# Kernel optimization log

Measured on AMD Instinct MI355X. Metric: run time of the kernel, lower is better.

The kernel has to match this reference:

```python
import jax, jax.numpy as jnp
import numpy as np

D_MODEL = 2048
D_LATENT = 512


def setup_inputs() -> dict:
    key = jax.random.key(0)
    ks = jax.random.split(key, 6)
    x = jax.random.normal(ks[0], (2, 4096, D_MODEL), dtype=jnp.float32)
    cache = jax.random.normal(ks[1], (2, 4096, D_LATENT), dtype=jnp.float32)
    s = 0.02
    # weights stored (in_features, out_features); equivalent to torch Linear (no bias)
    W_kv = jax.random.normal(ks[2], (D_MODEL, D_LATENT), dtype=jnp.float32) * s
    W_q = jax.random.normal(ks[3], (D_MODEL, D_MODEL), dtype=jnp.float32) * s
    W_lq = jax.random.normal(ks[4], (D_MODEL, D_LATENT), dtype=jnp.float32) * s
    W_o = jax.random.normal(ks[5], (D_LATENT, D_MODEL), dtype=jnp.float32) * s
    return {"x": x, "cache": cache, "W_kv": W_kv, "W_q": W_q, "W_lq": W_lq, "W_o": W_o}


def reference(x, cache, W_kv, W_q, W_lq, W_o):
    # latent compression of inputs: (B, S, d_latent)
    l_kv_new = jnp.einsum('bsd,dl->bsl', x, W_kv)
    # query path: x -> query (d_model) -> latent query (d_latent)
    q = jnp.einsum('bsd,de->bse', x, W_q)
    lq = jnp.einsum('bse,el->bsl', q, W_lq)
    # append to cache: (B, T+S, d_latent)
    l_kv = jnp.concatenate([cache, l_kv_new], axis=1)
    scale = jnp.sqrt(jnp.float32(D_LATENT)).astype(x.dtype)
    # attention in latent space: scores (B, S, T+S)
    scores = jnp.einsum('bsl,btl->bst', lq, l_kv) / scale
    weights = jax.nn.softmax(scores, axis=-1)
    ctx = jnp.einsum('bst,btl->bsl', weights, l_kv)
    out = jnp.einsum('bsl,ld->bsd', ctx, W_o)
    return out, l_kv
```

## Files before the change

### kernel.cpp

```cpp
#include <hip/hip_runtime.h>
#include <hip/hip_bf16.h>
#include <math.h>


typedef _Float16 f16x8 __attribute__((ext_vector_type(8)));
typedef _Float16 f16x4 __attribute__((ext_vector_type(4)));
typedef float    f32x4 __attribute__((ext_vector_type(4)));
typedef float    f32x8 __attribute__((ext_vector_type(8)));

__device__ __forceinline__ void gl_lds16(const void* g, void* l) {
  __builtin_amdgcn_global_load_lds(
      (const __attribute__((address_space(1))) void*)g,
      (__attribute__((address_space(3))) void*)l, 16, 0, 0);
}


__global__ __launch_bounds__(256) void k_cvt(const float* __restrict__ in,
                                             _Float16* __restrict__ out, int n4) {
  int i = blockIdx.x * blockDim.x + threadIdx.x;
  int st = gridDim.x * blockDim.x;
  for (; i < n4; i += st) {
    f32x4 v = reinterpret_cast<const f32x4*>(in)[i];
    reinterpret_cast<f16x4*>(out)[i] = __builtin_convertvector(v, f16x4);
  }
}

__global__ __launch_bounds__(256) void k_cache(const float* __restrict__ cache,
                                               float* __restrict__ lkv_f32,
                                               _Float16* __restrict__ lkv16, int n4) {
  int i = blockIdx.x * blockDim.x + threadIdx.x;
  int st = gridDim.x * blockDim.x;
  for (; i < n4; i += st) {
    f32x4 v = reinterpret_cast<const f32x4*>(cache)[i];
    int e = i << 2;
    int b = e >> 21;
    int dst = e + (b << 21);
    *reinterpret_cast<f32x4*>(lkv_f32 + dst) = v;
    *reinterpret_cast<f16x4*>(lkv16 + dst) = __builtin_convertvector(v, f16x4);
  }
}

__global__ __launch_bounds__(256) void k_tc(const float* __restrict__ in,
                                            _Float16* __restrict__ out, int R, int C) {
  __shared__ float t[32][33];
  const int c0 = blockIdx.x << 5, r0 = blockIdx.y << 5;
  const int tid = threadIdx.x;
  {
    int r = tid >> 3, c4 = (tid & 7) << 2;
    f32x4 v = *reinterpret_cast<const f32x4*>(&in[(long)(r0 + r) * C + c0 + c4]);
    t[r][c4] = v[0]; t[r][c4 + 1] = v[1]; t[r][c4 + 2] = v[2]; t[r][c4 + 3] = v[3];
  }
  __syncthreads();
  {
    int c = tid >> 3, r4 = (tid & 7) << 2;
    f16x4 o = {(_Float16)t[r4][c], (_Float16)t[r4 + 1][c],
               (_Float16)t[r4 + 2][c], (_Float16)t[r4 + 3][c]};
    *reinterpret_cast<f16x4*>(&out[(long)(c0 + c) * R + r0 + r4]) = o;
  }
}

__global__ __launch_bounds__(256) void k_tb(const _Float16* __restrict__ in,
                                            _Float16* __restrict__ out, int R, int C) {
  __shared__ _Float16 t[32][36];
  const int c0 = blockIdx.x << 5, r0 = blockIdx.y << 5;
  const int tid = threadIdx.x;
  {
    int r = tid >> 3, c4 = (tid & 7) << 2;
    f16x4 v = *reinterpret_cast<const f16x4*>(&in[(long)(r0 + r) * C + c0 + c4]);
    t[r][c4] = v[0]; t[r][c4 + 1] = v[1]; t[r][c4 + 2] = v[2]; t[r][c4 + 3] = v[3];
  }
  __syncthreads();
  {
    int c = tid >> 3, r4 = (tid & 7) << 2;
    f16x4 o = {t[r4][c], t[r4 + 1][c], t[r4 + 2][c], t[r4 + 3][c]};
    *reinterpret_cast<f16x4*>(&out[(long)(c0 + c) * R + r0 + r4]) = o;
  }
}

template <int CMODE>
__global__ __launch_bounds__(256) void k_gemm(const _Float16* __restrict__ A,
                                              const _Float16* __restrict__ B,
                                              float* __restrict__ Cf,
                                              _Float16* __restrict__ Ch,
                                              int M, int N, int K, int lda, int ldb,
                                              float cscale) {
  if constexpr (CMODE == 4) {
    const long z = blockIdx.z;
    A += z * K;
    B += z * K;
    Cf += z * (long)M * N;
  }
  __shared__ alignas(16) _Float16 As[128 * 64];
  __shared__ alignas(16) _Float16 Bs[128 * 64];
  const int tid = threadIdx.x;
  const int lane = tid & 63;
  const int w = tid >> 6;
  const int wr = ((w >> 1) & 1) << 6, wc = (w & 1) << 6;
  const int bm = blockIdx.x << 7, bn = blockIdx.y << 7;
  const int g = lane >> 4, ln15 = lane & 15;

  f32x4 acc[4][4] = {};

  const int srowl = lane >> 3;
  const int skcol = (lane & 7) << 3;
  const int wofs = (srowl << 6) + (((lane & 7) ^ srowl) << 3);

  f16x8 ra[4], rb[4];
  auto loadregs = [&](int k0) {
#pragma unroll
    for (int i = 0; i < 4; ++i) {
      int ch = (w << 2) + i;
      int row = (ch << 3) + srowl;
      ra[i] = *reinterpret_cast<const f16x8*>(&A[(long)(bm + row) * lda + k0 + skcol]);
      rb[i] = *reinterpret_cast<const f16x8*>(&B[(long)(bn + row) * ldb + k0 + skcol]);
    }
  };
  loadregs(0);
  const int nk = K >> 6;
  for (int kt = 0; kt < nk; ++kt) {
    __syncthreads();
#pragma unroll
    for (int i = 0; i < 4; ++i) {
      int ch = (w << 2) + i;
      *reinterpret_cast<f16x8*>(&As[(ch << 9) + wofs]) = ra[i];
      *reinterpret_cast<f16x8*>(&Bs[(ch << 9) + wofs]) = rb[i];
    }
    __syncthreads();
    if (kt + 1 < nk) loadregs((kt + 1) << 6);
#pragma unroll
    for (int ks = 0; ks < 2; ++ks) {
      f16x8 af[4], bf[4];
#pragma unroll
      for (int i = 0; i < 4; ++i) {
        const int arow = wr + (i << 4) + ln15;
        const int brow = wc + (i << 4) + ln15;
        const int inner = (((ks << 5) + (g << 3)) ^ ((ln15 & 7) << 3));
        af[i] = *reinterpret_cast<const f16x8*>(&As[arow * 64 + inner]);
        bf[i] = *reinterpret_cast<const f16x8*>(&Bs[brow * 64 + inner]);
      }
#pragma unroll
      for (int i = 0; i < 4; ++i)
#pragma unroll
        for (int j = 0; j < 4; ++j)
          acc[i][j] = __builtin_amdgcn_mfma_f32_16x16x32_f16(af[i], bf[j], acc[i][j], 0, 0, 0);
    }
  }
#pragma unroll
  for (int i = 0; i < 4; ++i) {
    const int row = bm + wr + (i << 4) + (g << 2);
#pragma unroll
    for (int j = 0; j < 4; ++j) {
      const int col = bn + wc + (j << 4) + ln15;
#pragma unroll
      for (int r = 0; r < 4; ++r) {
        float v = acc[i][j][r];
        long orow = row + r;
        if constexpr (CMODE == 2) {
          long m2 = ((orow >> 12) << 13) + 4096 + (orow & 4095);
          Cf[m2 * 512 + col] = v;
          Ch[m2 * 512 + col] = (_Float16)v;
        } else if constexpr (CMODE == 1) {
          Ch[orow * N + col] = (_Float16)v;
        } else if constexpr (CMODE == 3) {
          Ch[orow * N + col] = (_Float16)(v * cscale);
        } else {
          Cf[orow * N + col] = v;
        }
      }
    }
  }
}

template <int CMODE>
__global__ __launch_bounds__(512, 2) void k_gemm256(const _Float16* __restrict__ A,
                                                    const _Float16* __restrict__ B,
                                                    float* __restrict__ Cf,
                                                    _Float16* __restrict__ Ch,
                                                    int M, int N, int K,
                                                    int lda, int ldb) {
  extern __shared__ _Float16 sm[];
  _Float16* As = sm;
  _Float16* Bs = sm + 32768;
  const int tid = threadIdx.x;
  const int lane = tid & 63;
  const int w = tid >> 6;
  const int wm = w >> 2, wn = w & 3;
  const int bm = blockIdx.x << 8, bn = blockIdx.y << 8;
  const int g = lane >> 4, ln15 = lane & 15;

  f32x4 acc[8][4] = {};

  const int lrow8 = lane >> 3;
  const int lswz  = ((lane & 7) ^ lrow8) << 3;
  const _Float16* Ap[4];
  const _Float16* Bp[4];
  int loff[4];
#pragma unroll
  for (int i = 0; i < 4; ++i) {
    const int row = (i << 6) + (w << 3) + lrow8;
    Ap[i] = &A[(long)(bm + row) * lda + lswz];
    Bp[i] = &B[(long)(bn + row) * ldb + lswz];
    loff[i] = ((i << 6) + (w << 3)) << 6;
  }

  auto stage = [&](int buf, int kt) {
    const int k0 = kt << 6;
    const int bo = buf << 14;
#pragma unroll
    for (int i = 0; i < 4; ++i) {
      gl_lds16(Ap[i] + k0, &As[bo + loff[i]]);
      gl_lds16(Bp[i] + k0, &Bs[bo + loff[i]]);
    }
  };

  const int nk = K >> 6;
  stage(0, 0);
  if (nk > 1) stage(1, 1);

  for (int kt = 0; kt < nk; ++kt) {
    if (kt + 1 < nk) asm volatile("s_waitcnt vmcnt(8)" ::: "memory");
    else             asm volatile("s_waitcnt vmcnt(0)" ::: "memory");
    __builtin_amdgcn_sched_barrier(0);
    __builtin_amdgcn_s_barrier();
    const int bo = (kt & 1) << 14;
#pragma unroll
    for (int ks = 0; ks < 2; ++ks) {
      f16x8 af[8], bf[4];
      const int innersw = ((ks << 5) + (g << 3)) ^ ((ln15 & 7) << 3);
#pragma unroll
      for (int i = 0; i < 8; ++i) {
        const int arow = (wm << 7) + (i << 4) + ln15;
        af[i] = *reinterpret_cast<const f16x8*>(&As[bo + arow * 64 + innersw]);
      }
#pragma unroll
      for (int j = 0; j < 4; ++j) {
        const int brow = (wn << 6) + (j << 4) + ln15;
        bf[j] = *reinterpret_cast<const f16x8*>(&Bs[bo + brow * 64 + innersw]);
      }
#pragma unroll
      for (int i = 0; i < 8; ++i)
#pragma unroll
        for (int j = 0; j < 4; ++j)
          acc[i][j] = __builtin_amdgcn_mfma_f32_16x16x32_f16(af[i], bf[j], acc[i][j], 0, 0, 0);
    }
    asm volatile("s_waitcnt lgkmcnt(0)" ::: "memory");
    __builtin_amdgcn_sched_barrier(0);
    __builtin_amdgcn_s_barrier();
    if (kt + 2 < nk) stage(kt & 1, kt + 2);
  }

#pragma unroll
  for (int i = 0; i < 8; ++i) {
    const int row = bm + (wm << 7) + (i << 4) + (g << 2);
#pragma unroll
    for (int j = 0; j < 4; ++j) {
      const int col = bn + (wn << 6) + (j << 4) + ln15;
#pragma unroll
      for (int r = 0; r < 4; ++r) {
        if constexpr (CMODE == 1)
          Ch[(long)(row + r) * N + col] = (_Float16)acc[i][j][r];
        else
          Cf[(long)(row + r) * N + col] = acc[i][j][r];
      }
    }
  }
}

__global__ __launch_bounds__(256) void k_red4(const float* __restrict__ p,
                                              _Float16* __restrict__ o,
                                              int n4, float scale) {
  const f32x4* pv = reinterpret_cast<const f32x4*>(p);
  int i = blockIdx.x * blockDim.x + threadIdx.x;
  int st = gridDim.x * blockDim.x;
  for (; i < n4; i += st) {
    f32x4 a = pv[i] + pv[i + n4] + pv[i + 2 * n4] + pv[i + 3 * n4];
    a *= scale;
    reinterpret_cast<f16x4*>(o)[i] = __builtin_convertvector(a, f16x4);
  }
}

__global__ __launch_bounds__(256) void k_smax(_Float16* __restrict__ S) {
  const int tid = threadIdx.x;
  _Float16* row = S + ((long)blockIdx.x << 13);
  __shared__ float red[4];
  f16x8 v[4];
#pragma unroll
  for (int c = 0; c < 4; ++c)
    v[c] = *reinterpret_cast<const f16x8*>(row + (c << 11) + (tid << 3));
  float mx = -1e30f;
#pragma unroll
  for (int c = 0; c < 4; ++c) {
    f32x8 f = __builtin_convertvector(v[c], f32x8);
#pragma unroll
    for (int j = 0; j < 8; ++j) mx = fmaxf(mx, f[j]);
  }
#pragma unroll
  for (int o = 32; o > 0; o >>= 1) mx = fmaxf(mx, __shfl_xor(mx, o));
  if ((tid & 63) == 0) red[tid >> 6] = mx;
  __syncthreads();
  mx = fmaxf(fmaxf(red[0], red[1]), fmaxf(red[2], red[3]));
  float sum = 0.f;
  f32x8 p0, p1, p2, p3;
  {
    f32x8 f;
#define SMAX_EXP(PC, CI)                                         \
    f = __builtin_convertvector(v[CI], f32x8);                   \
    _Pragma("unroll")                                            \
    for (int j = 0; j < 8; ++j) { PC[j] = __expf(f[j] - mx); sum += PC[j]; }
    SMAX_EXP(p0, 0) SMAX_EXP(p1, 1) SMAX_EXP(p2, 2) SMAX_EXP(p3, 3)
#undef SMAX_EXP
  }
#pragma unroll
  for (int o = 32; o > 0; o >>= 1) sum += __shfl_xor(sum, o);
  __syncthreads();
  if ((tid & 63) == 0) red[tid >> 6] = sum;
  __syncthreads();
  const float inv = 1.f / (red[0] + red[1] + red[2] + red[3]);
  *reinterpret_cast<f16x8*>(row + (0 << 11) + (tid << 3)) = __builtin_convertvector(p0 * inv, f16x8);
  *reinterpret_cast<f16x8*>(row + (1 << 11) + (tid << 3)) = __builtin_convertvector(p1 * inv, f16x8);
  *reinterpret_cast<f16x8*>(row + (2 << 11) + (tid << 3)) = __builtin_convertvector(p2 * inv, f16x8);
  *reinterpret_cast<f16x8*>(row + (3 << 11) + (tid << 3)) = __builtin_convertvector(p3 * inv, f16x8);
}


extern "C" void kernel_launch(void* const* d_in, const int* in_sizes, int n_in,
                              void* d_out, int out_size, void* d_ws, size_t ws_size,
                              hipStream_t stream) {
  const float* x     = (const float*)d_in[0];
  const float* cache = (const float*)d_in[1];
  const float* W_kv  = (const float*)d_in[2];
  const float* W_q   = (const float*)d_in[3];
  const float* W_lq  = (const float*)d_in[4];
  const float* W_o   = (const float*)d_in[5];

  float* out     = (float*)d_out;
  float* lkv_out = out + (size_t)8192 * 2048;

  _Float16* base16 = (_Float16*)d_out;
  _Float16* x16    = base16;
  _Float16* lq16   = base16 + 16777216;
  _Float16* Wq16   = base16 + 20971520;
  _Float16* WlqT   = base16 + 25165824;
  _Float16* WcombT = base16 + 26214400;
  _Float16* WkvT   = base16 + 27262976;
  _Float16* lkvT16 = base16 + 20971520;
  float*    PVp    = (float*)d_out;

  _Float16* lkv16 = (_Float16*)d_ws;
  _Float16* ctx   = lkv16 + 8388608;
  _Float16* WoT   = ctx + 4194304;
  _Float16* Sbuf  = WoT + 1048576;
  float*    Wcp   = (float*)Sbuf;

  const size_t sbase = 27262976;
  int CR = 1024;
  if (ws_size >= sbase + (size_t)4096 * 8192 * 2) CR = 4096;
  else if (ws_size >= sbase + (size_t)2048 * 8192 * 2) CR = 2048;

  const float iscale = 0.044194173824159216f;

  hipFuncSetAttribute((const void*)k_gemm256<1>,
                      hipFuncAttributeMaxDynamicSharedMemorySize, 131072);
  hipFuncSetAttribute((const void*)k_gemm256<0>,
                      hipFuncAttributeMaxDynamicSharedMemorySize, 131072);

  k_cvt<<<1024, 256, 0, stream>>>(x, x16, 16777216 / 4);
  k_cache<<<1024, 256, 0, stream>>>(cache, lkv_out, lkv16, 4194304 / 4);
  k_tc<<<dim3(16, 64), 256, 0, stream>>>(W_kv, WkvT, 2048, 512);
  k_cvt<<<1024, 256, 0, stream>>>(W_q, Wq16, 4194304 / 4);
  k_tc<<<dim3(16, 64), 256, 0, stream>>>(W_lq, WlqT, 2048, 512);
  k_tc<<<dim3(64, 16), 256, 0, stream>>>(W_o, WoT, 512, 2048);

  k_gemm<2><<<dim3(64, 4), 256, 0, stream>>>(x16, WkvT, lkv_out, lkv16,
                                             8192, 512, 2048, 2048, 2048, 1.f);
  k_gemm<4><<<dim3(4, 16, 4), 256, 0, stream>>>(WlqT, Wq16, Wcp, nullptr,
                                                512, 2048, 512, 2048, 2048, 1.f);
  k_red4<<<1024, 256, 0, stream>>>(Wcp, WcombT, (512 * 2048) / 4, iscale);
  k_gemm<1><<<dim3(64, 4), 256, 0, stream>>>(x16, WcombT, nullptr, lq16,
                                             8192, 512, 2048, 2048, 2048, 1.f);
  k_tb<<<dim3(16, 512), 256, 0, stream>>>(lkv16, lkvT16, 16384, 512);

  for (long r0 = 0; r0 < 8192; r0 += CR) {
    const long b = r0 >> 12;
    k_gemm256<1><<<dim3(CR >> 8, 32), 512, 131072, stream>>>(
        lq16 + r0 * 512, lkv16 + b * 8192 * 512, nullptr, Sbuf,
        CR, 8192, 512, 512, 512);
    k_smax<<<CR, 256, 0, stream>>>(Sbuf);
    k_gemm<4><<<dim3(CR >> 7, 4, 4), 256, 0, stream>>>(
        Sbuf, lkvT16 + b * 8192, PVp, nullptr,
        CR, 512, 2048, 8192, 16384, 1.f);
    k_red4<<<2048, 256, 0, stream>>>(PVp, ctx + r0 * 512, (CR * 512) / 4, 1.f);
  }

  k_gemm256<0><<<dim3(32, 8), 512, 131072, stream>>>(ctx, WoT, out, nullptr,
                                                     8192, 2048, 512, 512, 512);
}
```

Baseline: 375.7 us.

## Fuse softmax into QK and PV GEMMs and merge latent projections

Removes the standalone softmax pass over the score matrix. The QK GEMM epilogue now emits per-row partial sums of exp(score), a small kernel turns them into reciprocal row sums, the PV GEMM applies exp to the score tile as it loads it, and the final split-K reduction scales each row by its reciprocal sum. Separately, the kv-latent and lq projections become one GEMM of width 1024 over the adjacent concatenated weights, with an epilogue that routes each half to its outputs. This saves a full read and write of the large fp16 score buffer and one pass over x, but drops the max subtraction, so exp can saturate (clamped at 60000) when scores are large, and exp is recomputed for every N block of the PV GEMM.

```diff
diff --git a/kernel.cpp b/kernel.cpp
--- a/kernel.cpp
+++ b/kernel.cpp
@@ -82,9 +82,10 @@
                                               const _Float16* __restrict__ B,
                                               float* __restrict__ Cf,
                                               _Float16* __restrict__ Ch,
+                                              _Float16* __restrict__ Ch2,
                                               int M, int N, int K, int lda, int ldb,
                                               float cscale) {
-  if constexpr (CMODE == 4) {
+  if constexpr (CMODE == 4 || CMODE == 6) {
     const long z = blockIdx.z;
     A += z * K;
     B += z * K;
@@ -113,6 +114,12 @@
       int row = (ch << 3) + srowl;
       ra[i] = *reinterpret_cast<const f16x8*>(&A[(long)(bm + row) * lda + k0 + skcol]);
       rb[i] = *reinterpret_cast<const f16x8*>(&B[(long)(bn + row) * ldb + k0 + skcol]);
+      if constexpr (CMODE == 6) {
+        f32x8 t = __builtin_convertvector(ra[i], f32x8);
+#pragma unroll
+        for (int j = 0; j < 8; ++j) t[j] = fminf(__expf(t[j]), 60000.f);
+        ra[i] = __builtin_convertvector(t, f16x8);
+      }
     }
   };
   loadregs(0);
@@ -163,6 +170,14 @@
           Ch[orow * N + col] = (_Float16)v;
         } else if constexpr (CMODE == 3) {
           Ch[orow * N + col] = (_Float16)(v * cscale);
+        } else if constexpr (CMODE == 5) {
+          if (col < 512) {
+            Ch[orow * 512 + col] = (_Float16)v;
+          } else {
+            long m2 = ((orow >> 12) << 13) + 4096 + (orow & 4095);
+            Cf[m2 * 512 + (col - 512)] = v;
+            Ch2[m2 * 512 + (col - 512)] = (_Float16)v;
+          }
         } else {
           Cf[orow * N + col] = v;
         }
@@ -171,11 +186,12 @@
   }
 }
 
-template <int CMODE>
+template <int CMODE, int STATS>
 __global__ __launch_bounds__(512, 2) void k_gemm256(const _Float16* __restrict__ A,
                                                     const _Float16* __restrict__ B,
                                                     float* __restrict__ Cf,
                                                     _Float16* __restrict__ Ch,
+                                                    float* __restrict__ Lp,
                                                     int M, int N, int K,
                                                     int lda, int ldb) {
   extern __shared__ _Float16 sm[];
@@ -264,6 +280,46 @@
       }
     }
   }
+
+  if constexpr (STATS) {
+    float* Lsh = (float*)sm;
+    float part[8][4];
+#pragma unroll
+    for (int i = 0; i < 8; ++i)
+#pragma unroll
+      for (int r = 0; r < 4; ++r) {
+        float s = 0.f;
+#pragma unroll
+        for (int j = 0; j < 4; ++j)
+          s += __expf((float)(_Float16)acc[i][j][r]);
+#pragma unroll
+        for (int off = 1; off < 16; off <<= 1) s += __shfl_xor(s, off);
+        part[i][r] = s;
+      }
+    if (ln15 == 0) {
+#pragma unroll
+      for (int i = 0; i < 8; ++i)
+#pragma unroll
+        for (int r = 0; r < 4; ++r) {
+          const int lrow = (wm << 7) + (i << 4) + (g << 2) + r;
+          Lsh[(lrow << 2) + wn] = part[i][r];
+        }
+    }
+    __syncthreads();
+    if (tid < 256) {
+      float L = Lsh[(tid << 2)] + Lsh[(tid << 2) + 1] +
+                Lsh[(tid << 2) + 2] + Lsh[(tid << 2) + 3];
+      Lp[(long)(bm + tid) * gridDim.y + blockIdx.y] = L;
+    }
+  }
+}
+
+__global__ __launch_bounds__(256) void k_linv(const float* __restrict__ Lp,
+                                              float* __restrict__ Linv, int nb) {
+  const int r = (blockIdx.x << 8) + threadIdx.x;
+  float s = 0.f;
+  for (int i = 0; i < nb; ++i) s += Lp[(long)r * nb + i];
+  Linv[r] = 1.f / s;
 }
 
 __global__ __launch_bounds__(256) void k_red4(const float* __restrict__ p,
@@ -279,47 +335,17 @@
   }
 }
 
-__global__ __launch_bounds__(256) void k_smax(_Float16* __restrict__ S) {
-  const int tid = threadIdx.x;
-  _Float16* row = S + ((long)blockIdx.x << 13);
-  __shared__ float red[4];
-  f16x8 v[4];
-#pragma unroll
-  for (int c = 0; c < 4; ++c)
-    v[c] = *reinterpret_cast<const f16x8*>(row + (c << 11) + (tid << 3));
-  float mx = -1e30f;
-#pragma unroll
-  for (int c = 0; c < 4; ++c) {
-    f32x8 f = __builtin_convertvector(v[c], f32x8);
-#pragma unroll
-    for (int j = 0; j < 8; ++j) mx = fmaxf(mx, f[j]);
-  }
-#pragma unroll
-  for (int o = 32; o > 0; o >>= 1) mx = fmaxf(mx, __shfl_xor(mx, o));
-  if ((tid & 63) == 0) red[tid >> 6] = mx;
-  __syncthreads();
-  mx = fmaxf(fmaxf(red[0], red[1]), fmaxf(red[2], red[3]));
-  float sum = 0.f;
-  f32x8 p0, p1, p2, p3;
-  {
-    f32x8 f;
-#define SMAX_EXP(PC, CI)                                         \
-    f = __builtin_convertvector(v[CI], f32x8);                   \
-    _Pragma("unroll")                                            \
-    for (int j = 0; j < 8; ++j) { PC[j] = __expf(f[j] - mx); sum += PC[j]; }
-    SMAX_EXP(p0, 0) SMAX_EXP(p1, 1) SMAX_EXP(p2, 2) SMAX_EXP(p3, 3)
-#undef SMAX_EXP
-  }
-#pragma unroll
-  for (int o = 32; o > 0; o >>= 1) sum += __shfl_xor(sum, o);
-  __syncthreads();
-  if ((tid & 63) == 0) red[tid >> 6] = sum;
-  __syncthreads();
-  const float inv = 1.f / (red[0] + red[1] + red[2] + red[3]);
-  *reinterpret_cast<f16x8*>(row + (0 << 11) + (tid << 3)) = __builtin_convertvector(p0 * inv, f16x8);
-  *reinterpret_cast<f16x8*>(row + (1 << 11) + (tid << 3)) = __builtin_convertvector(p1 * inv, f16x8);
-  *reinterpret_cast<f16x8*>(row + (2 << 11) + (tid << 3)) = __builtin_convertvector(p2 * inv, f16x8);
-  *reinterpret_cast<f16x8*>(row + (3 << 11) + (tid << 3)) = __builtin_convertvector(p3 * inv, f16x8);
+__global__ __launch_bounds__(256) void k_red4row(const float* __restrict__ p,
+                                                 const float* __restrict__ Linv,
+                                                 _Float16* __restrict__ o, int n4) {
+  const f32x4* pv = reinterpret_cast<const f32x4*>(p);
+  int i = blockIdx.x * blockDim.x + threadIdx.x;
+  int st = gridDim.x * blockDim.x;
+  for (; i < n4; i += st) {
+    f32x4 a = pv[i] + pv[i + n4] + pv[i + 2 * n4] + pv[i + 3 * n4];
+    a *= Linv[i >> 7];
+    reinterpret_cast<f16x4*>(o)[i] = __builtin_convertvector(a, f16x4);
+  }
 }
 
 
@@ -345,6 +371,8 @@
   _Float16* WkvT   = base16 + 27262976;
   _Float16* lkvT16 = base16 + 20971520;
   float*    PVp    = (float*)d_out;
+  float*    Lp     = (float*)(base16 + 29360128);
+  float*    Linv   = Lp + 131072;
 
   _Float16* lkv16 = (_Float16*)d_ws;
   _Float16* ctx   = lkv16 + 8388608;
@@ -359,9 +387,9 @@
 
   const float iscale = 0.044194173824159216f;
 
-  hipFuncSetAttribute((const void*)k_gemm256<1>,
+  hipFuncSetAttribute((const void*)k_gemm256<1, 1>,
                       hipFuncAttributeMaxDynamicSharedMemorySize, 131072);
-  hipFuncSetAttribute((const void*)k_gemm256<0>,
+  hipFuncSetAttribute((const void*)k_gemm256<0, 0>,
                       hipFuncAttributeMaxDynamicSharedMemorySize, 131072);
 
   k_cvt<<<1024, 256, 0, stream>>>(x, x16, 16777216 / 4);
@@ -371,27 +399,26 @@
   k_tc<<<dim3(16, 64), 256, 0, stream>>>(W_lq, WlqT, 2048, 512);
   k_tc<<<dim3(64, 16), 256, 0, stream>>>(W_o, WoT, 512, 2048);
 
-  k_gemm<2><<<dim3(64, 4), 256, 0, stream>>>(x16, WkvT, lkv_out, lkv16,
-                                             8192, 512, 2048, 2048, 2048, 1.f);
-  k_gemm<4><<<dim3(4, 16, 4), 256, 0, stream>>>(WlqT, Wq16, Wcp, nullptr,
+  k_gemm<4><<<dim3(4, 16, 4), 256, 0, stream>>>(WlqT, Wq16, Wcp, nullptr, nullptr,
                                                 512, 2048, 512, 2048, 2048, 1.f);
   k_red4<<<1024, 256, 0, stream>>>(Wcp, WcombT, (512 * 2048) / 4, iscale);
-  k_gemm<1><<<dim3(64, 4), 256, 0, stream>>>(x16, WcombT, nullptr, lq16,
-                                             8192, 512, 2048, 2048, 2048, 1.f);
+  k_gemm<5><<<dim3(64, 8), 256, 0, stream>>>(x16, WcombT, lkv_out, lq16, lkv16,
+                                             8192, 1024, 2048, 2048, 2048, 1.f);
   k_tb<<<dim3(16, 512), 256, 0, stream>>>(lkv16, lkvT16, 16384, 512);
 
   for (long r0 = 0; r0 < 8192; r0 += CR) {
     const long b = r0 >> 12;
-    k_gemm256<1><<<dim3(CR >> 8, 32), 512, 131072, stream>>>(
-        lq16 + r0 * 512, lkv16 + b * 8192 * 512, nullptr, Sbuf,
+    k_gemm256<1, 1><<<dim3(CR >> 8, 32), 512, 131072, stream>>>(
+        lq16 + r0 * 512, lkv16 + b * 8192 * 512, nullptr, Sbuf, Lp,
         CR, 8192, 512, 512, 512);
-    k_smax<<<CR, 256, 0, stream>>>(Sbuf);
-    k_gemm<4><<<dim3(CR >> 7, 4, 4), 256, 0, stream>>>(
-        Sbuf, lkvT16 + b * 8192, PVp, nullptr,
+    k_linv<<<CR >> 8, 256, 0, stream>>>(Lp, Linv, 32);
+    k_gemm<6><<<dim3(CR >> 7, 4, 4), 256, 0, stream>>>(
+        Sbuf, lkvT16 + b * 8192, PVp, nullptr, nullptr,
         CR, 512, 2048, 8192, 16384, 1.f);
-    k_red4<<<2048, 256, 0, stream>>>(PVp, ctx + r0 * 512, (CR * 512) / 4, 1.f);
-  }
-
-  k_gemm256<0><<<dim3(32, 8), 512, 131072, stream>>>(ctx, WoT, out, nullptr,
-                                                     8192, 2048, 512, 512, 512);
-}
+    k_red4row<<<2048, 256, 0, stream>>>(PVp, Linv, ctx + r0 * 512, (CR * 512) / 4);
+  }
+
+  k_gemm256<0, 0><<<dim3(32, 8), 512, 131072, stream>>>(ctx, WoT, out, nullptr,
+                                                        nullptr,
+                                                        8192, 2048, 512, 512, 512);
+}
```

Result: no change. 375.6 us (-0.0%).
